# Kernel tuning notes

Measured on AMD Instinct MI355X. Metric: run time of the kernel, lower is better.

Reference implementation:

```python
import jax, jax.numpy as jnp
import numpy as np

EPS = 1e-05


def setup_inputs() -> dict:
    key = jax.random.key(0)
    k1, = jax.random.split(key, 1)
    B = 16
    SEG = 62500  # points per cloud
    N = B * SEG  # 1,000,000 total points
    D = 128
    x_x = jax.random.normal(k1, (N, D), dtype=jnp.float32)
    seqlen = (jnp.arange(B + 1, dtype=jnp.int32) * SEG)  # cumulative offsets [B+1]
    weight = jnp.ones((1, D), dtype=jnp.float32)
    bias = jnp.zeros((1, D), dtype=jnp.float32)
    return {"x_x": x_x, "seqlen": seqlen, "weight": weight, "bias": bias}


def reference(x_x, seqlen, weight, bias):
    N, D = x_x.shape
    B = seqlen.shape[0] - 1
    # seqlen_to_batch_index: bidx[i] = segment containing point i
    bidx = jnp.searchsorted(seqlen, jnp.arange(N, dtype=seqlen.dtype), side="right") - 1
    counts = (seqlen[1:] - seqlen[:-1]).astype(x_x.dtype)  # [B]
    denom = jnp.maximum(counts, 1.0)[:, None]  # scatter_mean clamps empty segs
    # scatter_mean of x over segments -> per-cloud mean [B, D]
    mean = jax.ops.segment_sum(x_x, bidx, num_segments=B) / denom
    x_hat = x_x - mean[bidx]  # gather-broadcast back to points
    # scatter_mean of centered squares -> per-cloud variance [B, D]
    var = jax.ops.segment_sum(x_hat * x_hat, bidx, num_segments=B) / denom
    std = jnp.sqrt(var + EPS)
    x_hat = x_hat / std[bidx]
    x_hat = x_hat * weight + bias  # affine=True
    return x_hat
```

## Files before the change

### kernel.cpp

```cpp
#include <hip/hip_runtime.h>

#define EPS 1e-5f
#define D4 32

typedef float __attribute__((ext_vector_type(4))) f32x4;

__global__ __launch_bounds__(256) void pin_stats_kernel(
    const float* __restrict__ x, const int* __restrict__ seqlen,
    float* __restrict__ gsum, float* __restrict__ gsq) {
    const int b = blockIdx.y;
    const int start = seqlen[b];
    const int rows = seqlen[b + 1] - start;
    const int c4 = threadIdx.x & 31;
    const int rg = threadIdx.x >> 5;

    f32x4 sum = 0.f;
    f32x4 sq  = 0.f;
    const f32x4* xp = (const f32x4*)x + (size_t)start * D4;
    const int rstride = gridDim.x * 8;
    const size_t pstep = (size_t)rstride * D4;

    int r = blockIdx.x * 8 + rg;
    const f32x4* p = xp + (size_t)r * D4 + c4;
    for (; r + rstride < rows; r += 2 * rstride, p += 2 * pstep) {
        f32x4 v0 = p[0];
        f32x4 v1 = p[pstep];
        sum += v0; sq += v0 * v0;
        sum += v1; sq += v1 * v1;
    }
    if (r < rows) {
        f32x4 v = p[0];
        sum += v; sq += v * v;
    }

    __shared__ f32x4 ssum[256];
    __shared__ f32x4 ssq[256];
    ssum[threadIdx.x] = sum;
    ssq[threadIdx.x]  = sq;
    __syncthreads();

    if (threadIdx.x < 32) {
        f32x4 ts = ssum[threadIdx.x];
        f32x4 tq = ssq[threadIdx.x];
        #pragma unroll
        for (int g = 1; g < 8; ++g) {
            ts += ssum[g * 32 + threadIdx.x];
            tq += ssq[g * 32 + threadIdx.x];
        }
        float* gs = gsum + b * 128 + threadIdx.x * 4;
        float* gq = gsq  + b * 128 + threadIdx.x * 4;
        atomicAdd(gs + 0, ts.x); atomicAdd(gs + 1, ts.y);
        atomicAdd(gs + 2, ts.z); atomicAdd(gs + 3, ts.w);
        atomicAdd(gq + 0, tq.x); atomicAdd(gq + 1, tq.y);
        atomicAdd(gq + 2, tq.z); atomicAdd(gq + 3, tq.w);
    }
}

__global__ __launch_bounds__(256) void pin_norm_kernel(
    const float* __restrict__ x, const int* __restrict__ seqlen,
    const float* __restrict__ gsum, const float* __restrict__ gsq,
    const float* __restrict__ weight, const float* __restrict__ bias,
    float* __restrict__ out) {
    const int b = blockIdx.y;
    const int start = seqlen[b];
    const int rows = seqlen[b + 1] - start;
    const int c4 = threadIdx.x & 31;
    const int rg = threadIdx.x >> 5;
    const int d = c4 * 4;

    const float inv_n = 1.0f / fmaxf((float)rows, 1.0f);
    f32x4 s  = *(const f32x4*)(gsum + b * 128 + d);
    f32x4 q  = *(const f32x4*)(gsq  + b * 128 + d);
    f32x4 w  = *(const f32x4*)(weight + d);
    f32x4 bi = *(const f32x4*)(bias + d);

    f32x4 m   = s * inv_n;
    f32x4 var = q * inv_n - m * m;
    f32x4 is;
    is.x = rsqrtf(var.x + EPS);
    is.y = rsqrtf(var.y + EPS);
    is.z = rsqrtf(var.z + EPS);
    is.w = rsqrtf(var.w + EPS);
    f32x4 scale = w * is;
    f32x4 shift = bi - m * scale;

    const f32x4* xp = (const f32x4*)x + (size_t)start * D4;
    f32x4* op = (f32x4*)out + (size_t)start * D4;
    const int rstride = gridDim.x * 8;
    const size_t pstep = (size_t)rstride * D4;

    int r = blockIdx.x * 8 + rg;
    size_t idx = (size_t)r * D4 + c4;
    for (; r + rstride < rows; r += 2 * rstride, idx += 2 * pstep) {
        f32x4 v0 = __builtin_nontemporal_load(xp + idx);
        f32x4 v1 = __builtin_nontemporal_load(xp + idx + pstep);
        f32x4 o0 = v0 * scale + shift;
        f32x4 o1 = v1 * scale + shift;
        __builtin_nontemporal_store(o0, op + idx);
        __builtin_nontemporal_store(o1, op + idx + pstep);
    }
    if (r < rows) {
        f32x4 v = __builtin_nontemporal_load(xp + idx);
        __builtin_nontemporal_store(v * scale + shift, op + idx);
    }
}

extern "C" void kernel_launch(void* const* d_in, const int* in_sizes, int n_in,
                              void* d_out, int out_size, void* d_ws, size_t ws_size,
                              hipStream_t stream) {
    const float* x      = (const float*)d_in[0];
    const int*   seqlen = (const int*)d_in[1];
    const float* weight = (const float*)d_in[2];
    const float* bias   = (const float*)d_in[3];
    float* out = (float*)d_out;

    const int B = in_sizes[1] - 1;
    float* gsum = (float*)d_ws;
    float* gsq  = gsum + (size_t)B * 128;

    hipMemsetAsync(d_ws, 0, (size_t)B * 128 * 2 * sizeof(float), stream);

    dim3 block(256);
    dim3 grid1(128, B);
    pin_stats_kernel<<<grid1, block, 0, stream>>>(x, seqlen, gsum, gsq);

    dim3 grid2(128, B);
    pin_norm_kernel<<<grid2, block, 0, stream>>>(x, seqlen, gsum, gsq, weight, bias, out);
}
```

Measured before the change: 883.7 us.

## Fuse stats and normalize into one cooperative kernel with reverse-order second pass

Merges the statistics and normalization kernels into a single cooperative kernel separated by a grid-wide sync. Each block now owns a contiguous chunk of rows and walks it backwards in the second pass, so the rows it read most recently are likely still in L2/MALL when re-read. The goal is to remove the second launch and cut the DRAM re-read of the 512MB input. The cost is a grid barrier and a smaller grid (64x16 blocks) that must be fully co-resident.

```diff
diff --git a/kernel.cpp b/kernel.cpp
--- a/kernel.cpp
+++ b/kernel.cpp
@@ -1,36 +1,45 @@
 #include <hip/hip_runtime.h>
+#include <hip/hip_cooperative_groups.h>
+
+namespace cg = cooperative_groups;
 
 #define EPS 1e-5f
 #define D4 32
 
 typedef float __attribute__((ext_vector_type(4))) f32x4;
 
-__global__ __launch_bounds__(256) void pin_stats_kernel(
+__global__ __launch_bounds__(256, 4) void pin_fused_kernel(
     const float* __restrict__ x, const int* __restrict__ seqlen,
-    float* __restrict__ gsum, float* __restrict__ gsq) {
-    const int b = blockIdx.y;
+    float* __restrict__ gsum, float* __restrict__ gsq,
+    const float* __restrict__ weight, const float* __restrict__ bias,
+    float* __restrict__ out)
+{
+    const int b   = blockIdx.y;
+    const int bx  = blockIdx.x;
+    const int nbx = gridDim.x;
     const int start = seqlen[b];
-    const int rows = seqlen[b + 1] - start;
+    const int rows  = seqlen[b + 1] - start;
     const int c4 = threadIdx.x & 31;
     const int rg = threadIdx.x >> 5;
 
-    f32x4 sum = 0.f;
-    f32x4 sq  = 0.f;
+    const int c0 = (int)(((long long)rows * bx) / nbx);
+    const int c1 = (int)(((long long)rows * (bx + 1)) / nbx);
+
     const f32x4* xp = (const f32x4*)x + (size_t)start * D4;
-    const int rstride = gridDim.x * 8;
-    const size_t pstep = (size_t)rstride * D4;
 
-    int r = blockIdx.x * 8 + rg;
-    const f32x4* p = xp + (size_t)r * D4 + c4;
-    for (; r + rstride < rows; r += 2 * rstride, p += 2 * pstep) {
-        f32x4 v0 = p[0];
-        f32x4 v1 = p[pstep];
-        sum += v0; sq += v0 * v0;
-        sum += v1; sq += v1 * v1;
-    }
-    if (r < rows) {
-        f32x4 v = p[0];
-        sum += v; sq += v * v;
+    f32x4 sum = 0.f, sq = 0.f;
+    {
+        int r = c0 + rg;
+        for (; r + 8 < c1; r += 16) {
+            f32x4 v0 = xp[(size_t)r * D4 + c4];
+            f32x4 v1 = xp[(size_t)(r + 8) * D4 + c4];
+            sum += v0; sq += v0 * v0;
+            sum += v1; sq += v1 * v1;
+        }
+        if (r < c1) {
+            f32x4 v = xp[(size_t)r * D4 + c4];
+            sum += v; sq += v * v;
+        }
     }
 
     __shared__ f32x4 ssum[256];
@@ -54,21 +63,11 @@
         atomicAdd(gq + 0, tq.x); atomicAdd(gq + 1, tq.y);
         atomicAdd(gq + 2, tq.z); atomicAdd(gq + 3, tq.w);
     }
-}
-
-__global__ __launch_bounds__(256) void pin_norm_kernel(
-    const float* __restrict__ x, const int* __restrict__ seqlen,
-    const float* __restrict__ gsum, const float* __restrict__ gsq,
-    const float* __restrict__ weight, const float* __restrict__ bias,
-    float* __restrict__ out) {
-    const int b = blockIdx.y;
-    const int start = seqlen[b];
-    const int rows = seqlen[b + 1] - start;
-    const int c4 = threadIdx.x & 31;
-    const int rg = threadIdx.x >> 5;
-    const int d = c4 * 4;
+    __threadfence();
+    cg::this_grid().sync();
 
     const float inv_n = 1.0f / fmaxf((float)rows, 1.0f);
+    const int d = c4 * 4;
     f32x4 s  = *(const f32x4*)(gsum + b * 128 + d);
     f32x4 q  = *(const f32x4*)(gsq  + b * 128 + d);
     f32x4 w  = *(const f32x4*)(weight + d);
@@ -84,22 +83,30 @@
     f32x4 scale = w * is;
     f32x4 shift = bi - m * scale;
 
-    const f32x4* xp = (const f32x4*)x + (size_t)start * D4;
     f32x4* op = (f32x4*)out + (size_t)start * D4;
-    const int rstride = gridDim.x * 8;
-    const size_t pstep = (size_t)rstride * D4;
+    const int len = c1 - c0;
+    const int ng  = (len + 7) >> 3;
 
-    int r = blockIdx.x * 8 + rg;
-    size_t idx = (size_t)r * D4 + c4;
-    for (; r + rstride < rows; r += 2 * rstride, idx += 2 * pstep) {
-        f32x4 v0 = __builtin_nontemporal_load(xp + idx);
-        f32x4 v1 = __builtin_nontemporal_load(xp + idx + pstep);
-        f32x4 o0 = v0 * scale + shift;
-        f32x4 o1 = v1 * scale + shift;
-        __builtin_nontemporal_store(o0, op + idx);
-        __builtin_nontemporal_store(o1, op + idx + pstep);
+    int g = ng - 1;
+    if (g >= 0) {
+        int r = c0 + g * 8 + rg;
+        if (r < c1) {
+            size_t idx = (size_t)r * D4 + c4;
+            f32x4 v = __builtin_nontemporal_load(xp + idx);
+            __builtin_nontemporal_store(v * scale + shift, op + idx);
+        }
+        --g;
     }
-    if (r < rows) {
+    for (; g >= 1; g -= 2) {
+        size_t i0 = (size_t)(c0 + g * 8 + rg) * D4 + c4;
+        size_t i1 = i0 - (size_t)8 * D4;
+        f32x4 v0 = __builtin_nontemporal_load(xp + i0);
+        f32x4 v1 = __builtin_nontemporal_load(xp + i1);
+        __builtin_nontemporal_store(v0 * scale + shift, op + i0);
+        __builtin_nontemporal_store(v1 * scale + shift, op + i1);
+    }
+    if (g == 0) {
+        size_t idx = (size_t)(c0 + rg) * D4 + c4;
         f32x4 v = __builtin_nontemporal_load(xp + idx);
         __builtin_nontemporal_store(v * scale + shift, op + idx);
     }
@@ -121,9 +128,8 @@
     hipMemsetAsync(d_ws, 0, (size_t)B * 128 * 2 * sizeof(float), stream);
 
     dim3 block(256);
-    dim3 grid1(128, B);
-    pin_stats_kernel<<<grid1, block, 0, stream>>>(x, seqlen, gsum, gsq);
-
-    dim3 grid2(128, B);
-    pin_norm_kernel<<<grid2, block, 0, stream>>>(x, seqlen, gsum, gsq, weight, bias, out);
+    dim3 grid(64, B);
+    void* args[] = {(void*)&x, (void*)&seqlen, (void*)&gsum, (void*)&gsq,
+                    (void*)&weight, (void*)&bias, (void*)&out};
+    hipLaunchCooperativeKernel((void*)pin_fused_kernel, grid, block, args, 0, stream);
 }
```

Result: slower. 1.067 ms (+20.7%).
